# Performance work log

Hardware: AMD Instinct MI355X
Metric: run time of the kernel (lower is better)

## Reference

```python
import jax, jax.numpy as jnp
import numpy as np

N_NODES = 100000
N_EDGES = 3200000


def gcn_conv(x, row, col, W, n):
    # PyG GCNConv: x @ W, then D^{-1/2}(A+I)D^{-1/2} aggregation (self-loops added).
    h = x @ W  # [N, out]
    loop = jnp.arange(n)
    r = jnp.concatenate([row, loop])
    c = jnp.concatenate([col, loop])
    deg = jax.ops.segment_sum(jnp.ones_like(c, dtype=h.dtype), c, num_segments=n)
    dinv = jnp.where(deg > 0, jax.lax.rsqrt(deg), 0.0)
    norm = dinv[r] * dinv[c]  # [E+N]
    msg = h[r] * norm[:, None]  # gather + scale
    return jax.ops.segment_sum(msg, c, num_segments=n)  # scatter-add


def setup_inputs() -> dict:
    key = jax.random.key(0)
    k1, k2, k3, k4, k5 = jax.random.split(key, 5)
    x = jax.random.normal(k1, (N_NODES, 1), dtype=jnp.float32)
    edge_index = jax.random.randint(k2, (2, N_EDGES), 0, N_NODES, dtype=jnp.int64)
    W1 = jax.random.normal(k3, (1, 16), dtype=jnp.float32) * 0.5
    W2 = jax.random.normal(k4, (16, 16), dtype=jnp.float32) * 0.25
    W3 = jax.random.normal(k5, (16, 11), dtype=jnp.float32) * 0.25
    b = jnp.zeros((11,), dtype=jnp.float32)
    return {"x": x, "edge_index": edge_index, "W1": W1, "W2": W2, "W3": W3, "b": b}


def reference(x, edge_index, W1, W2, W3, b):
    n = x.shape[0]
    row, col = edge_index[0], edge_index[1]
    h = jax.nn.relu(gcn_conv(x, row, col, W1, n))
    h = jax.nn.relu(gcn_conv(h, row, col, W2, n))
    g = jnp.mean(h, axis=0).reshape(-1, 16)  # [1,16] graph readout
    out = (g @ W3).squeeze() + b  # [11]
    return out
```

## Files before the change

### kernel.cpp

```cpp
#include <hip/hip_runtime.h>

static constexpr int N = 100000;
static constexpr int E = 3200000;
static constexpr int BUKSHIFT = 8;
static constexpr int BUKSZ = 1 << BUKSHIFT;
static constexpr int BUKMASK = BUKSZ - 1;
static constexpr int NBUK = (N + BUKSZ - 1) / BUKSZ;
static constexpr int CAP = 12288;
static constexpr int SC_CHUNK = 16384;
static constexpr int SC_T = 1024;
static constexpr int SC_BLOCKS = (E + SC_CHUNK - 1) / SC_CHUNK;


__global__ void k_init(int* __restrict__ gofs) {
    int i = threadIdx.x;
    if (i < NBUK) gofs[i] = i * CAP;
}

__global__ __launch_bounds__(SC_T) void k_scatter(const int4* __restrict__ rows4,
                                                  const int4* __restrict__ cols4,
                                                  int* __restrict__ gofs,
                                                  int* __restrict__ binned) {
    __shared__ int hist[4][NBUK];
    __shared__ int cnt[512];
    __shared__ int lbase[NBUK];
    __shared__ int gbase[NBUK];
    __shared__ int stag[SC_CHUNK];

    const int tid = threadIdx.x;
    const int g = tid >> 8;
    for (int i = tid; i < 4 * NBUK; i += SC_T) (&hist[0][0])[i] = 0;
    if (tid < 512) cnt[tid] = 0;
    __syncthreads();

    const int nI4 = E / 4;
    const int base4 = blockIdx.x * (SC_CHUNK / 4);
    int4 r[4], c[4];
    bool vld[4];
    #pragma unroll
    for (int k = 0; k < 4; ++k) {
        int idx = base4 + k * SC_T + tid;
        vld[k] = idx < nI4;
        if (vld[k]) { r[k] = rows4[idx]; c[k] = cols4[idx]; }
    }
    #pragma unroll
    for (int k = 0; k < 4; ++k) if (vld[k]) {
        atomicAdd(&hist[g][c[k].x >> BUKSHIFT], 1);
        atomicAdd(&hist[g][c[k].y >> BUKSHIFT], 1);
        atomicAdd(&hist[g][c[k].z >> BUKSHIFT], 1);
        atomicAdd(&hist[g][c[k].w >> BUKSHIFT], 1);
    }
    __syncthreads();

    if (tid < NBUK) {
        int h0 = hist[0][tid], h1 = hist[1][tid], h2 = hist[2][tid], h3 = hist[3][tid];
        hist[0][tid] = 0; hist[1][tid] = h0; hist[2][tid] = h0 + h1; hist[3][tid] = h0 + h1 + h2;
        int cc = h0 + h1 + h2 + h3;
        cnt[tid] = cc;
        gbase[tid] = cc ? atomicAdd(&gofs[tid], cc) : 0;
    }
    __syncthreads();
    for (int off = 1; off < 512; off <<= 1) {
        int v = 0;
        if (tid < 512) { v = cnt[tid]; if (tid >= off) v += cnt[tid - off]; }
        __syncthreads();
        if (tid < 512) cnt[tid] = v;
        __syncthreads();
    }
    if (tid < NBUK) lbase[tid] = tid ? cnt[tid - 1] : 0;
    __syncthreads();

    #pragma unroll
    for (int k = 0; k < 4; ++k) if (vld[k]) {
        int b, off;
        b = c[k].x >> BUKSHIFT; off = atomicAdd(&hist[g][b], 1); stag[lbase[b] + off] = (r[k].x << BUKSHIFT) | (c[k].x & BUKMASK);
        b = c[k].y >> BUKSHIFT; off = atomicAdd(&hist[g][b], 1); stag[lbase[b] + off] = (r[k].y << BUKSHIFT) | (c[k].y & BUKMASK);
        b = c[k].z >> BUKSHIFT; off = atomicAdd(&hist[g][b], 1); stag[lbase[b] + off] = (r[k].z << BUKSHIFT) | (c[k].z & BUKMASK);
        b = c[k].w >> BUKSHIFT; off = atomicAdd(&hist[g][b], 1); stag[lbase[b] + off] = (r[k].w << BUKSHIFT) | (c[k].w & BUKMASK);
    }
    __syncthreads();

    const int eTot = min(SC_CHUNK, E - blockIdx.x * SC_CHUNK);
    int s = tid * 16;
    if (s < eTot) {
        int lo = 0, hi = NBUK - 1;
        while (lo < hi) { int mid = (lo + hi + 1) >> 1; if (lbase[mid] <= s) lo = mid; else hi = mid - 1; }
        int b = lo;
        const int e1 = min(s + 16, eTot);
        for (; s < e1; ++s) {
            while (b + 1 < NBUK && lbase[b + 1] <= s) ++b;
            binned[gbase[b] + (s - lbase[b])] = stag[s];
        }
    }
}

__global__ __launch_bounds__(1024) void k_deg(const int* __restrict__ binned,
                                              const int* __restrict__ gofs,
                                              const float* __restrict__ x,
                                              float* __restrict__ dinv,
                                              float* __restrict__ y1) {
    __shared__ int cnt[8][BUKSZ];
    const int tid = threadIdx.x;
    for (int i = tid; i < 8 * BUKSZ; i += 1024) (&cnt[0][0])[i] = 0;
    __syncthreads();
    const int b = blockIdx.x, g = tid >> 7;
    const int s0 = b * CAP;
    const int n = gofs[b] - s0;
    const int n4 = n >> 2;
    const int4* b4 = (const int4*)(binned + s0);
    for (int i = tid; i < n4; i += 1024) {
        int4 p = b4[i];
        atomicAdd(&cnt[g][p.x & BUKMASK], 1);
        atomicAdd(&cnt[g][p.y & BUKMASK], 1);
        atomicAdd(&cnt[g][p.z & BUKMASK], 1);
        atomicAdd(&cnt[g][p.w & BUKMASK], 1);
    }
    if (tid < (n & 3)) atomicAdd(&cnt[g][binned[s0 + (n4 << 2) + tid] & BUKMASK], 1);
    __syncthreads();
    if (tid < BUKSZ) {
        int v = (b << BUKSHIFT) + tid;
        if (v < N) {
            int c = 0;
            #pragma unroll
            for (int q = 0; q < 8; ++q) c += cnt[q][tid];
            float d = rsqrtf(1.0f + (float)c);
            dinv[v] = d;
            y1[v] = d * x[v];
        }
    }
}

__global__ __launch_bounds__(1024) void k_acc1(const int* __restrict__ binned,
                                               const int* __restrict__ gofs,
                                               const float* __restrict__ y1,
                                               const float* __restrict__ dinv,
                                               float* __restrict__ m) {
    __shared__ float acc[8][BUKSZ];
    const int tid = threadIdx.x;
    for (int i = tid; i < 8 * BUKSZ; i += 1024) (&acc[0][0])[i] = 0.f;
    __syncthreads();
    const int b = blockIdx.x, g = tid >> 7;
    const int s0 = b * CAP;
    const int n = gofs[b] - s0;
    const int n4 = n >> 2;
    const int4* b4 = (const int4*)(binned + s0);
    for (int i = tid; i < n4; i += 1024) {
        int4 p = b4[i];
        atomicAdd(&acc[g][p.x & BUKMASK], y1[p.x >> BUKSHIFT]);
        atomicAdd(&acc[g][p.y & BUKMASK], y1[p.y >> BUKSHIFT]);
        atomicAdd(&acc[g][p.z & BUKMASK], y1[p.z >> BUKSHIFT]);
        atomicAdd(&acc[g][p.w & BUKMASK], y1[p.w >> BUKSHIFT]);
    }
    if (tid < (n & 3)) {
        int p = binned[s0 + (n4 << 2) + tid];
        atomicAdd(&acc[g][p & BUKMASK], y1[p >> BUKSHIFT]);
    }
    __syncthreads();
    if (tid < BUKSZ) {
        int v = (b << BUKSHIFT) + tid;
        if (v < N) {
            float a = 0.f;
            #pragma unroll
            for (int q = 0; q < 8; ++q) a += acc[q][tid];
            float d = dinv[v];
            float s = d * a + d * y1[v];
            m[v] = d * s;
        }
    }
}

__global__ __launch_bounds__(1024) void k_acc2(const int* __restrict__ binned,
                                               const int* __restrict__ gofs,
                                               const float* __restrict__ m,
                                               const float* __restrict__ dinv,
                                               const float* __restrict__ W1,
                                               const float* __restrict__ W2,
                                               float* __restrict__ partials) {
    __shared__ float tp[8][BUKSZ], tn[8][BUKSZ];
    __shared__ float sP[16], sM[16], sAcc[16];
    const int tid = threadIdx.x;
    if (tid < 16) {
        float p = 0.f, q = 0.f;
        for (int k = 0; k < 16; ++k) {
            float w1 = W1[k];
            float w2 = W2[k * 16 + tid];
            p += fmaxf(w1, 0.f) * w2;
            q += fminf(w1, 0.f) * w2;
        }
        sP[tid] = p; sM[tid] = q; sAcc[tid] = 0.f;
    }
    for (int i = tid; i < 8 * BUKSZ; i += 1024) { (&tp[0][0])[i] = 0.f; (&tn[0][0])[i] = 0.f; }
    __syncthreads();
    const int b = blockIdx.x, g = tid >> 7;
    const int s0 = b * CAP;
    const int n = gofs[b] - s0;
    const int n4 = n >> 2;
    const int4* b4 = (const int4*)(binned + s0);
    for (int i = tid; i < n4; i += 1024) {
        int4 p = b4[i];
        float v0 = m[p.x >> BUKSHIFT], v1 = m[p.y >> BUKSHIFT];
        float v2 = m[p.z >> BUKSHIFT], v3 = m[p.w >> BUKSHIFT];
        atomicAdd(v0 >= 0.f ? &tp[g][p.x & BUKMASK] : &tn[g][p.x & BUKMASK], v0);
        atomicAdd(v1 >= 0.f ? &tp[g][p.y & BUKMASK] : &tn[g][p.y & BUKMASK], v1);
        atomicAdd(v2 >= 0.f ? &tp[g][p.z & BUKMASK] : &tn[g][p.z & BUKMASK], v2);
        atomicAdd(v3 >= 0.f ? &tp[g][p.w & BUKMASK] : &tn[g][p.w & BUKMASK], v3);
    }
    if (tid < (n & 3)) {
        int p = binned[s0 + (n4 << 2) + tid];
        float val = m[p >> BUKSHIFT];
        atomicAdd(val >= 0.f ? &tp[g][p & BUKMASK] : &tn[g][p & BUKMASK], val);
    }
    __syncthreads();
    float alpha = 0.f, beta = 0.f;
    if (tid < BUKSZ) {
        int v = (b << BUKSHIFT) + tid;
        if (v < N) {
            float a = 0.f, bb = 0.f;
            #pragma unroll
            for (int q = 0; q < 8; ++q) { a += tp[q][tid]; bb += tn[q][tid]; }
            float d = dinv[v], mv = m[v];
            alpha = d * a;
            beta  = d * bb;
            float self = d * mv;
            if (mv >= 0.f) alpha += self; else beta += self;
        }
    }
    const int lane = tid & 63;
    for (int j = 0; j < 16; ++j) {
        float h = fmaxf(alpha * sP[j] + beta * sM[j], 0.f);
        #pragma unroll
        for (int off = 32; off > 0; off >>= 1) h += __shfl_down(h, off);
        if (lane == 0 && h != 0.f) atomicAdd(&sAcc[j], h);
    }
    __syncthreads();
    if (tid < 16) partials[b * 16 + tid] = sAcc[tid];
}

__global__ void k_out(const float* __restrict__ partials, const float* __restrict__ W3,
                      const float* __restrict__ b, float* __restrict__ out) {
    __shared__ float s[16][16];
    int j = threadIdx.x & 15;
    int g = threadIdx.x >> 4;
    float acc = 0.f;
    for (int blk = g; blk < NBUK; blk += 16) acc += partials[blk * 16 + j];
    s[g][j] = acc;
    __syncthreads();
    if (threadIdx.x < 16) {
        float tot = 0.f;
        #pragma unroll
        for (int gg = 0; gg < 16; ++gg) tot += s[gg][threadIdx.x];
        s[0][threadIdx.x] = tot * (1.0f / (float)N);
    }
    __syncthreads();
    if (threadIdx.x < 11) {
        float acc2 = b[threadIdx.x];
        #pragma unroll
        for (int k = 0; k < 16; ++k) acc2 += s[0][k] * W3[k * 11 + threadIdx.x];
        out[threadIdx.x] = acc2;
    }
}

extern "C" void kernel_launch(void* const* d_in, const int* in_sizes, int n_in,
                              void* d_out, int out_size, void* d_ws, size_t ws_size,
                              hipStream_t stream) {
    const float* x  = (const float*)d_in[0];
    const int*   ei = (const int*)d_in[1];
    const float* W1 = (const float*)d_in[2];
    const float* W2 = (const float*)d_in[3];
    const float* W3 = (const float*)d_in[4];
    const float* b  = (const float*)d_in[5];
    float* out = (float*)d_out;

    int*   wsi      = (int*)d_ws;
    int*   binned   = wsi;
    float* dinv     = (float*)(wsi + (size_t)NBUK * CAP);
    float* y1       = dinv + N;
    float* m        = y1 + N;
    int*   gofs     = (int*)(m + N);
    float* partials = (float*)(gofs + NBUK);

    const int4* rows4 = (const int4*)ei;
    const int4* cols4 = (const int4*)(ei + E);

    k_init   <<<1, 512, 0, stream>>>(gofs);
    k_scatter<<<SC_BLOCKS, SC_T, 0, stream>>>(rows4, cols4, gofs, binned);
    k_deg    <<<NBUK, 1024, 0, stream>>>(binned, gofs, x, dinv, y1);
    k_acc1   <<<NBUK, 1024, 0, stream>>>(binned, gofs, y1, dinv, m);
    k_acc2   <<<NBUK, 1024, 0, stream>>>(binned, gofs, m, dinv, W1, W2, partials);
    k_out    <<<1, 256, 0, stream>>>(partials, W3, b, out);
}
```

Baseline: 110.6 us.

## Split bucket counters into padded per-group sub-buckets to cut global atomic contention

Each bucket now has 8 sub-bucket write cursors, spaced 16 ints apart so they sit on separate cache lines, and each scatter block picks its sub-bucket from its block index. The goal is to spread the global atomicAdd reservations in k_scatter, which previously all hit a single counter per bucket. The scatter chunk size is halved to 8192 edges, doubling the block count, and each consumer kernel now loops over the 8 sub-ranges. The risk is overflow: each sub-bucket holds a fixed 1536 entries, which leaves less slack than one shared 12288-entry bucket if the blocks' edges spread unevenly.

```diff
diff --git a/kernel.cpp b/kernel.cpp
--- a/kernel.cpp
+++ b/kernel.cpp
@@ -6,15 +6,21 @@
 static constexpr int BUKSZ = 1 << BUKSHIFT;
 static constexpr int BUKMASK = BUKSZ - 1;
 static constexpr int NBUK = (N + BUKSZ - 1) / BUKSZ;
-static constexpr int CAP = 12288;
-static constexpr int SC_CHUNK = 16384;
+static constexpr int NGRP = 8;
+static constexpr int SUBCAP = 1536;
+static constexpr int CAP = NGRP * SUBCAP;
+static constexpr int GSTRIDE = 16;
+static constexpr int SC_CHUNK = 8192;
 static constexpr int SC_T = 1024;
 static constexpr int SC_BLOCKS = (E + SC_CHUNK - 1) / SC_CHUNK;
 
 
 __global__ void k_init(int* __restrict__ gofs) {
-    int i = threadIdx.x;
-    if (i < NBUK) gofs[i] = i * CAP;
+    int i = blockIdx.x * blockDim.x + threadIdx.x;
+    if (i < NBUK * NGRP) {
+        int b = i / NGRP, g = i % NGRP;
+        gofs[i * GSTRIDE] = b * CAP + g * SUBCAP;
+    }
 }
 
 __global__ __launch_bounds__(SC_T) void k_scatter(const int4* __restrict__ rows4,
@@ -29,35 +35,39 @@
 
     const int tid = threadIdx.x;
     const int g = tid >> 8;
+    const int grp = blockIdx.x & (NGRP - 1);
     for (int i = tid; i < 4 * NBUK; i += SC_T) (&hist[0][0])[i] = 0;
     if (tid < 512) cnt[tid] = 0;
     __syncthreads();
 
     const int nI4 = E / 4;
     const int base4 = blockIdx.x * (SC_CHUNK / 4);
-    int4 r[4], c[4];
-    bool vld[4];
-    #pragma unroll
-    for (int k = 0; k < 4; ++k) {
-        int idx = base4 + k * SC_T + tid;
-        vld[k] = idx < nI4;
-        if (vld[k]) { r[k] = rows4[idx]; c[k] = cols4[idx]; }
-    }
-    #pragma unroll
-    for (int k = 0; k < 4; ++k) if (vld[k]) {
-        atomicAdd(&hist[g][c[k].x >> BUKSHIFT], 1);
-        atomicAdd(&hist[g][c[k].y >> BUKSHIFT], 1);
-        atomicAdd(&hist[g][c[k].z >> BUKSHIFT], 1);
-        atomicAdd(&hist[g][c[k].w >> BUKSHIFT], 1);
+    const int ia = base4 + tid, ib = base4 + 1024 + tid;
+    const bool va = ia < nI4, vb = ib < nI4;
+    int4 ra, ca, rb, cb;
+    if (va) { ra = rows4[ia]; ca = cols4[ia]; }
+    if (vb) { rb = rows4[ib]; cb = cols4[ib]; }
+
+    if (va) {
+        atomicAdd(&hist[g][ca.x >> BUKSHIFT], 1);
+        atomicAdd(&hist[g][ca.y >> BUKSHIFT], 1);
+        atomicAdd(&hist[g][ca.z >> BUKSHIFT], 1);
+        atomicAdd(&hist[g][ca.w >> BUKSHIFT], 1);
+    }
+    if (vb) {
+        atomicAdd(&hist[g][cb.x >> BUKSHIFT], 1);
+        atomicAdd(&hist[g][cb.y >> BUKSHIFT], 1);
+        atomicAdd(&hist[g][cb.z >> BUKSHIFT], 1);
+        atomicAdd(&hist[g][cb.w >> BUKSHIFT], 1);
     }
     __syncthreads();
 
     if (tid < NBUK) {
         int h0 = hist[0][tid], h1 = hist[1][tid], h2 = hist[2][tid], h3 = hist[3][tid];
         hist[0][tid] = 0; hist[1][tid] = h0; hist[2][tid] = h0 + h1; hist[3][tid] = h0 + h1 + h2;
-        int cc = h0 + h1 + h2 + h3;
-        cnt[tid] = cc;
-        gbase[tid] = cc ? atomicAdd(&gofs[tid], cc) : 0;
+        int c = h0 + h1 + h2 + h3;
+        cnt[tid] = c;
+        gbase[tid] = c ? atomicAdd(&gofs[(tid * NGRP + grp) * GSTRIDE], c) : 0;
     }
     __syncthreads();
     for (int off = 1; off < 512; off <<= 1) {
@@ -70,23 +80,29 @@
     if (tid < NBUK) lbase[tid] = tid ? cnt[tid - 1] : 0;
     __syncthreads();
 
-    #pragma unroll
-    for (int k = 0; k < 4; ++k) if (vld[k]) {
+    if (va) {
         int b, off;
-        b = c[k].x >> BUKSHIFT; off = atomicAdd(&hist[g][b], 1); stag[lbase[b] + off] = (r[k].x << BUKSHIFT) | (c[k].x & BUKMASK);
-        b = c[k].y >> BUKSHIFT; off = atomicAdd(&hist[g][b], 1); stag[lbase[b] + off] = (r[k].y << BUKSHIFT) | (c[k].y & BUKMASK);
-        b = c[k].z >> BUKSHIFT; off = atomicAdd(&hist[g][b], 1); stag[lbase[b] + off] = (r[k].z << BUKSHIFT) | (c[k].z & BUKMASK);
-        b = c[k].w >> BUKSHIFT; off = atomicAdd(&hist[g][b], 1); stag[lbase[b] + off] = (r[k].w << BUKSHIFT) | (c[k].w & BUKMASK);
+        b = ca.x >> BUKSHIFT; off = atomicAdd(&hist[g][b], 1); stag[lbase[b] + off] = (ra.x << BUKSHIFT) | (ca.x & BUKMASK);
+        b = ca.y >> BUKSHIFT; off = atomicAdd(&hist[g][b], 1); stag[lbase[b] + off] = (ra.y << BUKSHIFT) | (ca.y & BUKMASK);
+        b = ca.z >> BUKSHIFT; off = atomicAdd(&hist[g][b], 1); stag[lbase[b] + off] = (ra.z << BUKSHIFT) | (ca.z & BUKMASK);
+        b = ca.w >> BUKSHIFT; off = atomicAdd(&hist[g][b], 1); stag[lbase[b] + off] = (ra.w << BUKSHIFT) | (ca.w & BUKMASK);
+    }
+    if (vb) {
+        int b, off;
+        b = cb.x >> BUKSHIFT; off = atomicAdd(&hist[g][b], 1); stag[lbase[b] + off] = (rb.x << BUKSHIFT) | (cb.x & BUKMASK);
+        b = cb.y >> BUKSHIFT; off = atomicAdd(&hist[g][b], 1); stag[lbase[b] + off] = (rb.y << BUKSHIFT) | (cb.y & BUKMASK);
+        b = cb.z >> BUKSHIFT; off = atomicAdd(&hist[g][b], 1); stag[lbase[b] + off] = (rb.z << BUKSHIFT) | (cb.z & BUKMASK);
+        b = cb.w >> BUKSHIFT; off = atomicAdd(&hist[g][b], 1); stag[lbase[b] + off] = (rb.w << BUKSHIFT) | (cb.w & BUKMASK);
     }
     __syncthreads();
 
     const int eTot = min(SC_CHUNK, E - blockIdx.x * SC_CHUNK);
-    int s = tid * 16;
+    int s = tid * 8;
     if (s < eTot) {
         int lo = 0, hi = NBUK - 1;
         while (lo < hi) { int mid = (lo + hi + 1) >> 1; if (lbase[mid] <= s) lo = mid; else hi = mid - 1; }
         int b = lo;
-        const int e1 = min(s + 16, eTot);
+        const int e1 = min(s + 8, eTot);
         for (; s < e1; ++s) {
             while (b + 1 < NBUK && lbase[b + 1] <= s) ++b;
             binned[gbase[b] + (s - lbase[b])] = stag[s];
@@ -104,18 +120,20 @@
     for (int i = tid; i < 8 * BUKSZ; i += 1024) (&cnt[0][0])[i] = 0;
     __syncthreads();
     const int b = blockIdx.x, g = tid >> 7;
-    const int s0 = b * CAP;
-    const int n = gofs[b] - s0;
-    const int n4 = n >> 2;
-    const int4* b4 = (const int4*)(binned + s0);
-    for (int i = tid; i < n4; i += 1024) {
-        int4 p = b4[i];
-        atomicAdd(&cnt[g][p.x & BUKMASK], 1);
-        atomicAdd(&cnt[g][p.y & BUKMASK], 1);
-        atomicAdd(&cnt[g][p.z & BUKMASK], 1);
-        atomicAdd(&cnt[g][p.w & BUKMASK], 1);
-    }
-    if (tid < (n & 3)) atomicAdd(&cnt[g][binned[s0 + (n4 << 2) + tid] & BUKMASK], 1);
+    for (int sg = 0; sg < NGRP; ++sg) {
+        const int s0 = b * CAP + sg * SUBCAP;
+        const int n = gofs[(b * NGRP + sg) * GSTRIDE] - s0;
+        const int n4 = n >> 2;
+        const int4* b4 = (const int4*)(binned + s0);
+        for (int i = tid; i < n4; i += 1024) {
+            int4 p = b4[i];
+            atomicAdd(&cnt[g][p.x & BUKMASK], 1);
+            atomicAdd(&cnt[g][p.y & BUKMASK], 1);
+            atomicAdd(&cnt[g][p.z & BUKMASK], 1);
+            atomicAdd(&cnt[g][p.w & BUKMASK], 1);
+        }
+        if (tid < (n & 3)) atomicAdd(&cnt[g][binned[s0 + (n4 << 2) + tid] & BUKMASK], 1);
+    }
     __syncthreads();
     if (tid < BUKSZ) {
         int v = (b << BUKSHIFT) + tid;
@@ -140,20 +158,22 @@
     for (int i = tid; i < 8 * BUKSZ; i += 1024) (&acc[0][0])[i] = 0.f;
     __syncthreads();
     const int b = blockIdx.x, g = tid >> 7;
-    const int s0 = b * CAP;
-    const int n = gofs[b] - s0;
-    const int n4 = n >> 2;
-    const int4* b4 = (const int4*)(binned + s0);
-    for (int i = tid; i < n4; i += 1024) {
-        int4 p = b4[i];
-        atomicAdd(&acc[g][p.x & BUKMASK], y1[p.x >> BUKSHIFT]);
-        atomicAdd(&acc[g][p.y & BUKMASK], y1[p.y >> BUKSHIFT]);
-        atomicAdd(&acc[g][p.z & BUKMASK], y1[p.z >> BUKSHIFT]);
-        atomicAdd(&acc[g][p.w & BUKMASK], y1[p.w >> BUKSHIFT]);
-    }
-    if (tid < (n & 3)) {
-        int p = binned[s0 + (n4 << 2) + tid];
-        atomicAdd(&acc[g][p & BUKMASK], y1[p >> BUKSHIFT]);
+    for (int sg = 0; sg < NGRP; ++sg) {
+        const int s0 = b * CAP + sg * SUBCAP;
+        const int n = gofs[(b * NGRP + sg) * GSTRIDE] - s0;
+        const int n4 = n >> 2;
+        const int4* b4 = (const int4*)(binned + s0);
+        for (int i = tid; i < n4; i += 1024) {
+            int4 p = b4[i];
+            atomicAdd(&acc[g][p.x & BUKMASK], y1[p.x >> BUKSHIFT]);
+            atomicAdd(&acc[g][p.y & BUKMASK], y1[p.y >> BUKSHIFT]);
+            atomicAdd(&acc[g][p.z & BUKMASK], y1[p.z >> BUKSHIFT]);
+            atomicAdd(&acc[g][p.w & BUKMASK], y1[p.w >> BUKSHIFT]);
+        }
+        if (tid < (n & 3)) {
+            int p = binned[s0 + (n4 << 2) + tid];
+            atomicAdd(&acc[g][p & BUKMASK], y1[p >> BUKSHIFT]);
+        }
     }
     __syncthreads();
     if (tid < BUKSZ) {
@@ -192,23 +212,25 @@
     for (int i = tid; i < 8 * BUKSZ; i += 1024) { (&tp[0][0])[i] = 0.f; (&tn[0][0])[i] = 0.f; }
     __syncthreads();
     const int b = blockIdx.x, g = tid >> 7;
-    const int s0 = b * CAP;
-    const int n = gofs[b] - s0;
-    const int n4 = n >> 2;
-    const int4* b4 = (const int4*)(binned + s0);
-    for (int i = tid; i < n4; i += 1024) {
-        int4 p = b4[i];
-        float v0 = m[p.x >> BUKSHIFT], v1 = m[p.y >> BUKSHIFT];
-        float v2 = m[p.z >> BUKSHIFT], v3 = m[p.w >> BUKSHIFT];
-        atomicAdd(v0 >= 0.f ? &tp[g][p.x & BUKMASK] : &tn[g][p.x & BUKMASK], v0);
-        atomicAdd(v1 >= 0.f ? &tp[g][p.y & BUKMASK] : &tn[g][p.y & BUKMASK], v1);
-        atomicAdd(v2 >= 0.f ? &tp[g][p.z & BUKMASK] : &tn[g][p.z & BUKMASK], v2);
-        atomicAdd(v3 >= 0.f ? &tp[g][p.w & BUKMASK] : &tn[g][p.w & BUKMASK], v3);
-    }
-    if (tid < (n & 3)) {
-        int p = binned[s0 + (n4 << 2) + tid];
-        float val = m[p >> BUKSHIFT];
-        atomicAdd(val >= 0.f ? &tp[g][p & BUKMASK] : &tn[g][p & BUKMASK], val);
+    for (int sg = 0; sg < NGRP; ++sg) {
+        const int s0 = b * CAP + sg * SUBCAP;
+        const int n = gofs[(b * NGRP + sg) * GSTRIDE] - s0;
+        const int n4 = n >> 2;
+        const int4* b4 = (const int4*)(binned + s0);
+        for (int i = tid; i < n4; i += 1024) {
+            int4 p = b4[i];
+            float v0 = m[p.x >> BUKSHIFT], v1 = m[p.y >> BUKSHIFT];
+            float v2 = m[p.z >> BUKSHIFT], v3 = m[p.w >> BUKSHIFT];
+            atomicAdd(v0 >= 0.f ? &tp[g][p.x & BUKMASK] : &tn[g][p.x & BUKMASK], v0);
+            atomicAdd(v1 >= 0.f ? &tp[g][p.y & BUKMASK] : &tn[g][p.y & BUKMASK], v1);
+            atomicAdd(v2 >= 0.f ? &tp[g][p.z & BUKMASK] : &tn[g][p.z & BUKMASK], v2);
+            atomicAdd(v3 >= 0.f ? &tp[g][p.w & BUKMASK] : &tn[g][p.w & BUKMASK], v3);
+        }
+        if (tid < (n & 3)) {
+            int p = binned[s0 + (n4 << 2) + tid];
+            float val = m[p >> BUKSHIFT];
+            atomicAdd(val >= 0.f ? &tp[g][p & BUKMASK] : &tn[g][p & BUKMASK], val);
+        }
     }
     __syncthreads();
     float alpha = 0.f, beta = 0.f;
@@ -277,12 +299,12 @@
     float* y1       = dinv + N;
     float* m        = y1 + N;
     int*   gofs     = (int*)(m + N);
-    float* partials = (float*)(gofs + NBUK);
+    float* partials = (float*)(gofs + NBUK * NGRP * GSTRIDE);
 
     const int4* rows4 = (const int4*)ei;
     const int4* cols4 = (const int4*)(ei + E);
 
-    k_init   <<<1, 512, 0, stream>>>(gofs);
+    k_init   <<<(NBUK * NGRP + 511) / 512, 512, 0, stream>>>(gofs);
     k_scatter<<<SC_BLOCKS, SC_T, 0, stream>>>(rows4, cols4, gofs, binned);
     k_deg    <<<NBUK, 1024, 0, stream>>>(binned, gofs, x, dinv, y1);
     k_acc1   <<<NBUK, 1024, 0, stream>>>(binned, gofs, y1, dinv, m);
```

After: 108.3 us. 1.02x faster.
